# Optimization experiments

Measured on AMD Instinct MI355X. Metric: run time of the kernel, lower is better.

Reference implementation:

```python
import jax, jax.numpy as jnp
import numpy as np
import math


def setup_inputs() -> dict:
    key = jax.random.key(0)
    B, S, H, D = 4, 2048, 16, 64
    qkv = jax.random.normal(key, (B, S, 3, H, D), dtype=jnp.float32)
    return {"qkv": qkv}


def reference(qkv):
    # qkv: (B, S, 3, H, D)
    B, S, _, H, D = qkv.shape
    q = jnp.transpose(qkv[:, :, 0], (0, 2, 1, 3))  # (B, H, S, D)
    k = jnp.transpose(qkv[:, :, 1], (0, 2, 1, 3))
    v = jnp.transpose(qkv[:, :, 2], (0, 2, 1, 3))
    scale = 1.0 / math.sqrt(D)
    scores = scale * jnp.einsum('bhsd,bhtd->bhst', q, k)  # (B, H, S, S)
    causal_mask = jnp.triu(jnp.ones((S, S), dtype=bool), k=1)
    scores = jnp.where(causal_mask, -jnp.inf, scores)
    attn = jax.nn.softmax(scores, axis=-1)
    # dropout_p = 0.0 (and module in eval mode) -> identity
    out = jnp.einsum('bhst,bhtd->bhsd', attn, v)  # (B, H, S, D)
    out = jnp.transpose(out, (0, 2, 1, 3)).reshape(B, S, H * D)
    return out
```

## Files before the change

kernel.cpp:

```cpp
#include <hip/hip_runtime.h>
#include <hip/hip_bf16.h>

typedef unsigned short u16;
typedef __attribute__((ext_vector_type(8))) short short8;
typedef __attribute__((ext_vector_type(4))) float f32x4;

constexpr int SEQ = 2048;
constexpr int NH  = 16;
constexpr int HD  = 64;
constexpr float SCALE = 0.125f;

constexpr int KP = 72;
constexpr int PP = 72;

__device__ __forceinline__ f32x4 mfma16(short8 a, short8 b, f32x4 c) {
    return __builtin_amdgcn_mfma_f32_16x16x32_bf16(a, b, c, 0, 0, 0);
}

__device__ __forceinline__ u16 bf16r(float x) {
    __hip_bfloat16 h = __float2bfloat16(x);
    return *reinterpret_cast<u16*>(&h);
}

__device__ __forceinline__ short8 cv8(const float* p) {
    float4 a = *(const float4*)p;
    float4 b = *(const float4*)(p + 4);
    short8 r;
    r[0] = (short)bf16r(a.x); r[1] = (short)bf16r(a.y);
    r[2] = (short)bf16r(a.z); r[3] = (short)bf16r(a.w);
    r[4] = (short)bf16r(b.x); r[5] = (short)bf16r(b.y);
    r[6] = (short)bf16r(b.z); r[7] = (short)bf16r(b.w);
    return r;
}

__global__ __launch_bounds__(256, 4)
void attn_fwd_kernel(const float* __restrict__ qkv, float* __restrict__ out) {
    __shared__ u16 Ks[64 * KP];
    __shared__ u16 Vt[64 * 64];
    __shared__ u16 Ps[4][16 * PP];

    const int orig = blockIdx.x;
    const int v    = (orig & 7) * 128 + (orig >> 3);
    const int bh   = v >> 4;
    const int p    = v & 15;
    const int b    = bh >> 4;
    const int h    = bh & 15;
    const int qtT[2] = {p, 31 - p};

    const int tid  = threadIdx.x;
    const int wave = tid >> 6;
    const int lane = tid & 63;
    const int llo  = lane & 15;
    const int lhi  = lane >> 4;

    const int q0[2] = {qtT[0] * 64 + wave * 16, qtT[1] * 64 + wave * 16};

    const size_t basebh = (size_t)b * SEQ * 3072 + (size_t)h * HD;

    short8 qf[2][2];
#pragma unroll
    for (int t = 0; t < 2; ++t) {
        const float* qp = qkv + basebh + (size_t)(q0[t] + llo) * 3072 + lhi * 8;
        qf[t][0] = cv8(qp);
        qf[t][1] = cv8(qp + 32);
    }

    f32x4 acc[2][4] = {};
    float m_r[2][4], l_r[2][4];
#pragma unroll
    for (int t = 0; t < 2; ++t)
#pragma unroll
        for (int r = 0; r < 4; ++r) { m_r[t][r] = -INFINITY; l_r[t][r] = 0.f; }

    const int NT = 32 - p;
    for (int kt = 0; kt < NT; ++kt) {
        const int kbase = kt * 64;
        __syncthreads();
        {
            const int r   = tid >> 2;
            const int c16 = (tid & 3) * 16;
            const float* kp = qkv + basebh + (size_t)(kbase + r) * 3072 + 1024 + c16;
            *(short8*)(&Ks[r * KP + c16])     = cv8(kp);
            *(short8*)(&Ks[r * KP + c16 + 8]) = cv8(kp + 8);
        }
        {
            const int d  = tid & 63;
            const int rg = tid >> 6;
            const float* vp = qkv + basebh + (size_t)(kbase + rg * 16) * 3072 + 2048 + d;
#pragma unroll
            for (int g = 0; g < 2; ++g) {
                short8 pk;
#pragma unroll
                for (int j = 0; j < 8; ++j)
                    pk[j] = (short)bf16r(vp[(g * 8 + j) * 3072]);
                char* dst = (char*)Vt + d * 128 + ((rg * 32 + g * 16) ^ ((d & 7) << 4));
                *(short8*)dst = pk;
            }
        }
        __syncthreads();

#pragma unroll
        for (int t = 0; t < 2; ++t) {
            if (kbase > q0[t] + 15) continue;

            float pv4[4][4];
            float pmax[4];
#pragma unroll
            for (int r = 0; r < 4; ++r) pmax[r] = -INFINITY;
#pragma unroll
            for (int cg = 0; cg < 4; ++cg) {
                const u16* kb = &Ks[(cg * 16 + llo) * KP + lhi * 8];
                short8 kf0 = *(const short8*)(kb);
                short8 kf1 = *(const short8*)(kb + 32);
                f32x4 s = {0.f, 0.f, 0.f, 0.f};
                s = mfma16(qf[t][0], kf0, s);
                s = mfma16(qf[t][1], kf1, s);
                const int kj = kbase + cg * 16 + llo;
#pragma unroll
                for (int r = 0; r < 4; ++r) {
                    const int qi = q0[t] + lhi * 4 + r;
                    float sv = s[r] * SCALE;
                    sv = (kj > qi) ? -INFINITY : sv;
                    pv4[cg][r] = sv;
                    pmax[r] = fmaxf(pmax[r], sv);
                }
            }
#pragma unroll
            for (int off = 1; off < 16; off <<= 1)
#pragma unroll
                for (int r = 0; r < 4; ++r)
                    pmax[r] = fmaxf(pmax[r], __shfl_xor(pmax[r], off, 64));

            float alpha[4], psum[4];
#pragma unroll
            for (int r = 0; r < 4; ++r) {
                float mn = fmaxf(m_r[t][r], pmax[r]);
                alpha[r] = __expf(m_r[t][r] - mn);
                m_r[t][r] = mn;
                float s0 = 0.f;
#pragma unroll
                for (int cg = 0; cg < 4; ++cg) {
                    pv4[cg][r] = __expf(pv4[cg][r] - mn);
                    s0 += pv4[cg][r];
                }
                psum[r] = s0;
            }
#pragma unroll
            for (int off = 1; off < 16; off <<= 1)
#pragma unroll
                for (int r = 0; r < 4; ++r)
                    psum[r] += __shfl_xor(psum[r], off, 64);
#pragma unroll
            for (int r = 0; r < 4; ++r) l_r[t][r] = l_r[t][r] * alpha[r] + psum[r];
#pragma unroll
            for (int dc = 0; dc < 4; ++dc)
#pragma unroll
                for (int r = 0; r < 4; ++r)
                    acc[t][dc][r] *= alpha[r];

            u16* pw = Ps[wave];
#pragma unroll
            for (int cg = 0; cg < 4; ++cg)
#pragma unroll
                for (int r = 0; r < 4; ++r)
                    pw[(lhi * 4 + r) * PP + cg * 16 + llo] = bf16r(pv4[cg][r]);

#pragma unroll
            for (int ks = 0; ks < 2; ++ks) {
                short8 pf = *(const short8*)(&pw[llo * PP + ks * 32 + lhi * 8]);
#pragma unroll
                for (int dc = 0; dc < 4; ++dc) {
                    const char* vsrc = (const char*)Vt + (dc * 16 + llo) * 128 +
                                       ((ks * 64 + lhi * 16) ^ ((llo & 7) << 4));
                    short8 vf = *(const short8*)vsrc;
                    acc[t][dc] = mfma16(pf, vf, acc[t][dc]);
                }
            }
        }
    }

#pragma unroll
    for (int t = 0; t < 2; ++t)
#pragma unroll
        for (int dc = 0; dc < 4; ++dc)
#pragma unroll
            for (int r = 0; r < 4; ++r) {
                const int qi = q0[t] + lhi * 4 + r;
                const int d  = dc * 16 + llo;
                out[((size_t)b * SEQ + qi) * (NH * HD) + h * HD + d] = acc[t][dc][r] / l_r[t][r];
            }
}

extern "C" void kernel_launch(void* const* d_in, const int* in_sizes, int n_in,
                              void* d_out, int out_size, void* d_ws, size_t ws_size,
                              hipStream_t stream) {
    const float* qkv = (const float*)d_in[0];
    float* out = (float*)d_out;
    const int B = in_sizes[0] / (SEQ * 3 * NH * HD);
    dim3 grid(B * NH * 16);
    dim3 block(256);
    attn_fwd_kernel<<<grid, block, 0, stream>>>(qkv, out);
}
```

Measured before the change: 285.3 us.

## Prefetch next K/V tile into registers and interleave both query tiles' MFMAs

Global loads of the next K and V tiles are issued into registers right after the shared-memory stores, so their latency overlaps with the current tile's compute. The QK^T and PV loops for the two causal query tiles are merged, so each K and V fragment read from LDS feeds both tiles' MFMAs, with a per-tile P buffer. The P row pitch changes from 72 to 68. With that pitch, short8 reads of P are only 8-byte aligned, which may split the LDS accesses, and the extra prefetch registers put occupancy at risk.

```diff
diff --git a/kernel.cpp b/kernel.cpp
--- a/kernel.cpp
+++ b/kernel.cpp
@@ -11,7 +11,7 @@
 constexpr float SCALE = 0.125f;
 
 constexpr int KP = 72;
-constexpr int PP = 72;
+constexpr int PP = 68;
 
 __device__ __forceinline__ f32x4 mfma16(short8 a, short8 b, f32x4 c) {
     return __builtin_amdgcn_mfma_f32_16x16x32_bf16(a, b, c, 0, 0, 0);
@@ -22,9 +22,7 @@
     return *reinterpret_cast<u16*>(&h);
 }
 
-__device__ __forceinline__ short8 cv8(const float* p) {
-    float4 a = *(const float4*)p;
-    float4 b = *(const float4*)(p + 4);
+__device__ __forceinline__ short8 pack8(float4 a, float4 b) {
     short8 r;
     r[0] = (short)bf16r(a.x); r[1] = (short)bf16r(a.y);
     r[2] = (short)bf16r(a.z); r[3] = (short)bf16r(a.w);
@@ -37,7 +35,7 @@
 void attn_fwd_kernel(const float* __restrict__ qkv, float* __restrict__ out) {
     __shared__ u16 Ks[64 * KP];
     __shared__ u16 Vt[64 * 64];
-    __shared__ u16 Ps[4][16 * PP];
+    __shared__ u16 Ps[4][2][16 * PP];
 
     const int orig = blockIdx.x;
     const int v    = (orig & 7) * 128 + (orig >> 3);
@@ -45,7 +43,6 @@
     const int p    = v & 15;
     const int b    = bh >> 4;
     const int h    = bh & 15;
-    const int qtT[2] = {p, 31 - p};
 
     const int tid  = threadIdx.x;
     const int wave = tid >> 6;
@@ -53,16 +50,15 @@
     const int llo  = lane & 15;
     const int lhi  = lane >> 4;
 
-    const int q0[2] = {qtT[0] * 64 + wave * 16, qtT[1] * 64 + wave * 16};
-
+    const int q0[2] = { p * 64 + wave * 16, (31 - p) * 64 + wave * 16 };
     const size_t basebh = (size_t)b * SEQ * 3072 + (size_t)h * HD;
 
     short8 qf[2][2];
 #pragma unroll
     for (int t = 0; t < 2; ++t) {
         const float* qp = qkv + basebh + (size_t)(q0[t] + llo) * 3072 + lhi * 8;
-        qf[t][0] = cv8(qp);
-        qf[t][1] = cv8(qp + 32);
+        qf[t][0] = pack8(*(const float4*)qp,        *(const float4*)(qp + 4));
+        qf[t][1] = pack8(*(const float4*)(qp + 32), *(const float4*)(qp + 36));
     }
 
     f32x4 acc[2][4] = {};
@@ -71,57 +67,83 @@
     for (int t = 0; t < 2; ++t)
 #pragma unroll
         for (int r = 0; r < 4; ++r) { m_r[t][r] = -INFINITY; l_r[t][r] = 0.f; }
+
+    const int kr  = tid >> 2;
+    const int kc  = (tid & 3) * 16;
+    const int vd  = tid & 63;
+    const int vrg = tid >> 6;
+    const float* kpg = qkv + basebh + (size_t)kr * 3072 + 1024 + kc;
+    const float* vpg = qkv + basebh + (size_t)(vrg * 16) * 3072 + 2048 + vd;
+
+    float4 kA, kB, kC, kD;
+    float  vr[16];
+
+#define LOADK(KT) { const float* pk_ = kpg + (size_t)(KT) * 64 * 3072;          \
+        kA = *(const float4*)pk_;       kB = *(const float4*)(pk_ + 4);         \
+        kC = *(const float4*)(pk_ + 8); kD = *(const float4*)(pk_ + 12); }
+#define LOADV(KT) { const float* pv_ = vpg + (size_t)(KT) * 64 * 3072;          \
+        _Pragma("unroll") for (int j_ = 0; j_ < 16; ++j_) vr[j_] = pv_[j_ * 3072]; }
+
+    LOADK(0);
+    LOADV(0);
 
     const int NT = 32 - p;
     for (int kt = 0; kt < NT; ++kt) {
         const int kbase = kt * 64;
         __syncthreads();
+        *(short8*)&Ks[kr * KP + kc]     = pack8(kA, kB);
+        *(short8*)&Ks[kr * KP + kc + 8] = pack8(kC, kD);
         {
-            const int r   = tid >> 2;
-            const int c16 = (tid & 3) * 16;
-            const float* kp = qkv + basebh + (size_t)(kbase + r) * 3072 + 1024 + c16;
-            *(short8*)(&Ks[r * KP + c16])     = cv8(kp);
-            *(short8*)(&Ks[r * KP + c16 + 8]) = cv8(kp + 8);
-        }
-        {
-            const int d  = tid & 63;
-            const int rg = tid >> 6;
-            const float* vp = qkv + basebh + (size_t)(kbase + rg * 16) * 3072 + 2048 + d;
-#pragma unroll
-            for (int g = 0; g < 2; ++g) {
-                short8 pk;
-#pragma unroll
-                for (int j = 0; j < 8; ++j)
-                    pk[j] = (short)bf16r(vp[(g * 8 + j) * 3072]);
-                char* dst = (char*)Vt + d * 128 + ((rg * 32 + g * 16) ^ ((d & 7) << 4));
-                *(short8*)dst = pk;
-            }
+            short8 p0, p1;
+#pragma unroll
+            for (int j = 0; j < 8; ++j) {
+                p0[j] = (short)bf16r(vr[j]);
+                p1[j] = (short)bf16r(vr[8 + j]);
+            }
+            char* vb = (char*)Vt + vd * 128;
+            *(short8*)(vb + ((vrg * 32)      ^ ((vd & 7) << 4))) = p0;
+            *(short8*)(vb + ((vrg * 32 + 16) ^ ((vd & 7) << 4))) = p1;
         }
         __syncthreads();
+        if (kt + 1 < NT) LOADK(kt + 1);
+
+        const bool act0 = (kt <= p);
+
+        float pv[2][4][4];
+#pragma unroll
+        for (int cg = 0; cg < 4; ++cg) {
+            const u16* kb = &Ks[(cg * 16 + llo) * KP + lhi * 8];
+            short8 kf0 = *(const short8*)(kb);
+            short8 kf1 = *(const short8*)(kb + 32);
+            f32x4 s1 = {0.f, 0.f, 0.f, 0.f};
+            s1 = mfma16(qf[1][0], kf0, s1);
+            s1 = mfma16(qf[1][1], kf1, s1);
+#pragma unroll
+            for (int r = 0; r < 4; ++r) pv[1][cg][r] = s1[r];
+            if (act0) {
+                f32x4 s0 = {0.f, 0.f, 0.f, 0.f};
+                s0 = mfma16(qf[0][0], kf0, s0);
+                s0 = mfma16(qf[0][1], kf1, s0);
+#pragma unroll
+                for (int r = 0; r < 4; ++r) pv[0][cg][r] = s0[r];
+            }
+        }
 
 #pragma unroll
         for (int t = 0; t < 2; ++t) {
-            if (kbase > q0[t] + 15) continue;
-
-            float pv4[4][4];
+            if (t == 0 && !act0) continue;
             float pmax[4];
 #pragma unroll
             for (int r = 0; r < 4; ++r) pmax[r] = -INFINITY;
 #pragma unroll
             for (int cg = 0; cg < 4; ++cg) {
-                const u16* kb = &Ks[(cg * 16 + llo) * KP + lhi * 8];
-                short8 kf0 = *(const short8*)(kb);
-                short8 kf1 = *(const short8*)(kb + 32);
-                f32x4 s = {0.f, 0.f, 0.f, 0.f};
-                s = mfma16(qf[t][0], kf0, s);
-                s = mfma16(qf[t][1], kf1, s);
                 const int kj = kbase + cg * 16 + llo;
 #pragma unroll
                 for (int r = 0; r < 4; ++r) {
                     const int qi = q0[t] + lhi * 4 + r;
-                    float sv = s[r] * SCALE;
+                    float sv = pv[t][cg][r] * SCALE;
                     sv = (kj > qi) ? -INFINITY : sv;
-                    pv4[cg][r] = sv;
+                    pv[t][cg][r] = sv;
                     pmax[r] = fmaxf(pmax[r], sv);
                 }
             }
@@ -140,8 +162,8 @@
                 float s0 = 0.f;
 #pragma unroll
                 for (int cg = 0; cg < 4; ++cg) {
-                    pv4[cg][r] = __expf(pv4[cg][r] - mn);
-                    s0 += pv4[cg][r];
+                    pv[t][cg][r] = __expf(pv[t][cg][r] - mn);
+                    s0 += pv[t][cg][r];
                 }
                 psum[r] = s0;
             }
@@ -158,23 +180,28 @@
                 for (int r = 0; r < 4; ++r)
                     acc[t][dc][r] *= alpha[r];
 
-            u16* pw = Ps[wave];
+            u16* pw = Ps[wave][t];
 #pragma unroll
             for (int cg = 0; cg < 4; ++cg)
 #pragma unroll
                 for (int r = 0; r < 4; ++r)
-                    pw[(lhi * 4 + r) * PP + cg * 16 + llo] = bf16r(pv4[cg][r]);
-
-#pragma unroll
-            for (int ks = 0; ks < 2; ++ks) {
-                short8 pf = *(const short8*)(&pw[llo * PP + ks * 32 + lhi * 8]);
-#pragma unroll
-                for (int dc = 0; dc < 4; ++dc) {
-                    const char* vsrc = (const char*)Vt + (dc * 16 + llo) * 128 +
-                                       ((ks * 64 + lhi * 16) ^ ((llo & 7) << 4));
-                    short8 vf = *(const short8*)vsrc;
-                    acc[t][dc] = mfma16(pf, vf, acc[t][dc]);
-                }
+                    pw[(lhi * 4 + r) * PP + cg * 16 + llo] = bf16r(pv[t][cg][r]);
+        }
+
+        if (kt + 1 < NT) LOADV(kt + 1);
+
+#pragma unroll
+        for (int ks = 0; ks < 2; ++ks) {
+            short8 pf1 = *(const short8*)&Ps[wave][1][llo * PP + ks * 32 + lhi * 8];
+            short8 pf0 = pf1;
+            if (act0) pf0 = *(const short8*)&Ps[wave][0][llo * PP + ks * 32 + lhi * 8];
+#pragma unroll
+            for (int dc = 0; dc < 4; ++dc) {
+                const char* vsrc = (const char*)Vt + (dc * 16 + llo) * 128 +
+                                   ((ks * 64 + lhi * 16) ^ ((llo & 7) << 4));
+                short8 vf = *(const short8*)vsrc;
+                acc[1][dc] = mfma16(pf1, vf, acc[1][dc]);
+                if (act0) acc[0][dc] = mfma16(pf0, vf, acc[0][dc]);
             }
         }
     }
```

Result: slower. 924.4 us (+224.0%).
